# Optimization experiments

Measured on AMD Instinct MI355X. Metric: run time of the kernel, lower is better.

The kernel has to match this reference:

```python
import jax, jax.numpy as jnp
import numpy as np

N_NODES = 100000


def gcn_conv(x, edge_index, W, b, n_nodes):
    """PyG GCNConv: out = D^-1/2 (A + I) D^-1/2 (x @ W^T) + b."""
    src, dst = edge_index[0], edge_index[1]
    loop = jnp.arange(n_nodes, dtype=src.dtype)
    src = jnp.concatenate([src, loop])  # [E + N]
    dst = jnp.concatenate([dst, loop])
    # degree of each node as aggregation target (includes self loop)
    deg = jax.ops.segment_sum(jnp.ones_like(src, dtype=x.dtype), dst,
                              num_segments=n_nodes)
    deg_inv_sqrt = jnp.where(deg > 0, jax.lax.rsqrt(deg), 0.0)
    norm = deg_inv_sqrt[src] * deg_inv_sqrt[dst]  # [E + N]
    h = x @ W.T  # [N, out_dim]  (transform BEFORE propagate, as in PyG)
    msg = h[src] * norm[:, None]  # gather + scale  [E + N, out_dim]
    out = jax.ops.segment_sum(msg, dst, num_segments=n_nodes)  # scatter-add
    return out + b


def setup_inputs() -> dict:
    key = jax.random.key(0)
    k_x, k_e, k_w1, k_b1, k_w2, k_b2 = jax.random.split(key, 6)
    in_dim, hidden = 128, 16
    n_edges = 3200000
    x = jax.random.normal(k_x, (N_NODES, in_dim), dtype=jnp.float32)
    edge_index = jax.random.randint(k_e, (2, n_edges), 0, N_NODES,
                                    dtype=jnp.int64)
    # Glorot-ish init for the linear weights (PyG Linear stores [out, in])
    W1 = jax.random.normal(k_w1, (hidden, in_dim), dtype=jnp.float32) / np.sqrt(in_dim)
    b1 = jnp.zeros((hidden,), dtype=jnp.float32)
    W2 = jax.random.normal(k_w2, (1, hidden), dtype=jnp.float32) / np.sqrt(hidden)
    b2 = jnp.zeros((1,), dtype=jnp.float32)
    return {"x": x, "edge_index": edge_index,
            "W1": W1, "b1": b1, "W2": W2, "b2": b2}


def reference(x, edge_index, W1, b1, W2, b2):
    n = x.shape[0]
    h = jax.nn.relu(gcn_conv(x, edge_index, W1, b1, n))  # [N, hidden]
    out = gcn_conv(h, edge_index, W2, b2, n)  # [N, 1]
    return out.squeeze(-1)  # [N]
```

## Files before the change

kernel.cpp:

```cpp
#include <hip/hip_runtime.h>

#define IN_DIM 128
#define HID 16
#define BSHIFT 7
#define BMASK  127
#define BCAP   4864
#define MID    2432
#define PCH    8192
#define PTHR   512
#define EPT    (PCH / PTHR)
#define BTHR   512
#define TSCALE 4096.0f
#define ZSCALE 262144.0f

__global__ void init_kernel(const unsigned int* ei, int* flag, int* gcur) {
    int tid = blockIdx.x * blockDim.x + threadIdx.x;
    if (tid < 4096) gcur[tid] = 0;
    if (tid == 0) {
        int zeros = 0;
        for (int j = 0; j < 8; ++j)
            if (ei[2 * j + 1] == 0u) zeros++;
        *flag = (zeros >= 7) ? 1 : 0;
    }
}

__device__ __forceinline__ int edge_at(const void* ei, long long idx, int is64) {
    if (is64) return (int)((const long long*)ei)[idx];
    return ((const int*)ei)[idx];
}

__global__ __launch_bounds__(PTHR) void place_kernel(const void* ei, long long E,
        int* gcur, unsigned int* __restrict__ binned, int NB, const int* flag) {
    __shared__ int cnt[1024];
    __shared__ int wbase[1024];
    int tid = threadIdx.x;
    for (int i = tid; i < NB; i += PTHR) cnt[i] = 0;
    __syncthreads();
    const int is64 = *flag;
    const long long e0 = (long long)blockIdx.x * PCH;

    int sA[EPT], dA[EPT];
    if (e0 + PCH <= E) {
        if (is64) {
            const long long* p = (const long long*)ei;
#pragma unroll
            for (int j = 0; j < EPT; ++j) sA[j] = (int)p[e0 + j * PTHR + tid];
#pragma unroll
            for (int j = 0; j < EPT; ++j) dA[j] = (int)p[E + e0 + j * PTHR + tid];
        } else {
            const int* p = (const int*)ei;
#pragma unroll
            for (int j = 0; j < EPT; ++j) sA[j] = p[e0 + j * PTHR + tid];
#pragma unroll
            for (int j = 0; j < EPT; ++j) dA[j] = p[E + e0 + j * PTHR + tid];
        }
    } else {
#pragma unroll
        for (int j = 0; j < EPT; ++j) {
            long long e = e0 + j * PTHR + tid;
            bool ok = e < E;
            sA[j] = ok ? edge_at(ei, e, is64) : 0;
            dA[j] = ok ? edge_at(ei, E + e, is64) : -(BMASK + 1);
        }
    }

    unsigned int v[EPT];
    unsigned int br[EPT];
#pragma unroll
    for (int j = 0; j < EPT; ++j) {
        int b = dA[j] >> BSHIFT;
        bool ok = dA[j] >= 0;
        int r = ok ? atomicAdd(&cnt[b], 1) : 0;
        v[j]  = ((unsigned int)sA[j] << BSHIFT) | (unsigned int)(dA[j] & BMASK);
        br[j] = ok ? (((unsigned int)b << 16) | (unsigned int)r) : 0xFFFFFFFFu;
    }
    __syncthreads();
    const int q = (int)(blockIdx.x & 3);
    int* gc = gcur + q * 1024;
    for (int i = tid; i < NB; i += PTHR) {
        int c = cnt[i];
        wbase[i] = c ? atomicAdd(&gc[i], c) : 0;
    }
    __syncthreads();
    const int regBase = (q >> 1) * MID;
    const bool down = (q & 1);
#pragma unroll
    for (int j = 0; j < EPT; ++j) {
        if (br[j] != 0xFFFFFFFFu) {
            int b = (int)(br[j] >> 16);
            int r = (int)(br[j] & 0xFFFFu);
            int w = wbase[b] + r;
            if (w < MID) {
                int pos = regBase + (down ? (MID - 1 - w) : w);
                binned[(size_t)b * BCAP + pos] = v[j];
            }
        }
    }
}

__device__ __forceinline__ void bucket_ranges(const int* gcur, int b,
        int& r0hi, int& r1lo, int& r1hi, int& r2lo) {
    int cA = gcur[b];            if (cA > MID) cA = MID;
    int cB = gcur[1024 + b];     if (cB > MID - cA) cB = MID - cA;
    int cC = gcur[2048 + b];     if (cC > MID) cC = MID;
    int cD = gcur[3072 + b];     if (cD > MID - cC) cD = MID - cC;
    r0hi = cA;
    r1lo = MID - cB;
    r1hi = MID + cC;
    r2lo = BCAP - cD;
}

__global__ __launch_bounds__(BTHR) void degdis_kernel(
        const unsigned int* __restrict__ binned, const int* __restrict__ gcur,
        float* __restrict__ dis, int N) {
    __shared__ int cnt[128];
    int b = blockIdx.x, tid = threadIdx.x;
    int base = b * BCAP;
    int r0hi, r1lo, r1hi, r2lo;
    bucket_ranges(gcur, b, r0hi, r1lo, r1hi, r2lo);
    if (tid < 128) cnt[tid] = 0;
    __syncthreads();
    for (int e = tid; e < r0hi; e += BTHR)
        atomicAdd(&cnt[binned[(size_t)base + e] & BMASK], 1);
    for (int e = r1lo + tid; e < r1hi; e += BTHR)
        atomicAdd(&cnt[binned[(size_t)base + e] & BMASK], 1);
    for (int e = r2lo + tid; e < BCAP; e += BTHR)
        atomicAdd(&cnt[binned[(size_t)base + e] & BMASK], 1);
    __syncthreads();
    if (tid < 128) {
        int node = (b << BSHIFT) + tid;
        if (node < N) dis[node] = rsqrtf((float)(cnt[tid] + 1));
    }
}

__global__ __launch_bounds__(256) void gemm1_kernel(
        const float* __restrict__ x, const float* __restrict__ W1,
        const float* __restrict__ dis, short* __restrict__ ts16, int N) {
    __shared__ float red[4 * 64 * 17];
    const int tid = threadIdx.x;
    const int lane = tid & 63;
    const int wv = tid >> 6;
    const int wq = __builtin_amdgcn_readfirstlane(wv);
    const int n = blockIdx.x * 64 + lane;

    float acc[HID];
#pragma unroll
    for (int o = 0; o < HID; ++o) acc[o] = 0.f;

    if (n < N) {
        const float* xp = &x[(size_t)n * IN_DIM + wq * 32];
        float4 xv[8];
#pragma unroll
        for (int j = 0; j < 8; ++j) xv[j] = ((const float4*)xp)[j];
        const float* wp = &W1[wq * 32];
#pragma unroll
        for (int kk = 0; kk < 32; ++kk) {
            float xs = ((const float*)xv)[kk];
#pragma unroll
            for (int o = 0; o < HID; ++o)
                acc[o] = fmaf(xs, wp[(size_t)o * IN_DIM + kk], acc[o]);
        }
    }
#pragma unroll
    for (int o = 0; o < HID; ++o)
        red[(wv * 64 + lane) * 17 + o] = acc[o];
    __syncthreads();

    const int nl = tid >> 2;
    const int og = (tid & 3) * 4;
    const int nn = blockIdx.x * 64 + nl;
    if (nn < N) {
        float s0 = 0.f, s1 = 0.f, s2 = 0.f, s3 = 0.f;
#pragma unroll
        for (int w2 = 0; w2 < 4; ++w2) {
            const float* rp = &red[(w2 * 64 + nl) * 17 + og];
            s0 += rp[0]; s1 += rp[1]; s2 += rp[2]; s3 += rp[3];
        }
        float di = dis[nn] * TSCALE;
        int i0 = (int)rintf(fminf(fmaxf(di * s0, -32767.f), 32767.f));
        int i1 = (int)rintf(fminf(fmaxf(di * s1, -32767.f), 32767.f));
        int i2 = (int)rintf(fminf(fmaxf(di * s2, -32767.f), 32767.f));
        int i3 = (int)rintf(fminf(fmaxf(di * s3, -32767.f), 32767.f));
        uint2 pk;
        pk.x = ((unsigned int)i0 & 0xFFFFu) | ((unsigned int)i1 << 16);
        pk.y = ((unsigned int)i2 & 0xFFFFu) | ((unsigned int)i3 << 16);
        ((uint2*)ts16)[(size_t)nn * 4 + (tid & 3)] = pk;
    }
}

__global__ __launch_bounds__(BTHR) void agg1_kernel(
        const unsigned int* __restrict__ binned, const int* __restrict__ gcur,
        const short* __restrict__ ts16, const float* __restrict__ dis,
        const float* __restrict__ b1, const float* __restrict__ W2,
        float* __restrict__ zs, int N) {
    __shared__ int acc[128 * 17];
    int b = blockIdx.x, tid = threadIdx.x;
    for (int i = tid; i < 128 * 17; i += BTHR) acc[i] = 0;
    __syncthreads();
    int base = b * BCAP;
    int r0hi, r1lo, r1hi, r2lo;
    bucket_ranges(gcur, b, r0hi, r1lo, r1hi, r2lo);

#define AGG1_EDGE(IDX)                                                        \
    {                                                                         \
        unsigned int v = binned[(size_t)base + (IDX)];                        \
        int src = (int)(v >> BSHIFT);                                         \
        int row = (int)(v & BMASK) * 17;                                      \
        const int4* tp = (const int4*)(ts16 + (size_t)src * 16);              \
        int4 a = tp[0], c = tp[1];                                            \
        atomicAdd(&acc[row + 0],  (int)(short)(a.x & 0xFFFF));                \
        atomicAdd(&acc[row + 1],  a.x >> 16);                                 \
        atomicAdd(&acc[row + 2],  (int)(short)(a.y & 0xFFFF));                \
        atomicAdd(&acc[row + 3],  a.y >> 16);                                 \
        atomicAdd(&acc[row + 4],  (int)(short)(a.z & 0xFFFF));                \
        atomicAdd(&acc[row + 5],  a.z >> 16);                                 \
        atomicAdd(&acc[row + 6],  (int)(short)(a.w & 0xFFFF));                \
        atomicAdd(&acc[row + 7],  a.w >> 16);                                 \
        atomicAdd(&acc[row + 8],  (int)(short)(c.x & 0xFFFF));                \
        atomicAdd(&acc[row + 9],  c.x >> 16);                                 \
        atomicAdd(&acc[row + 10], (int)(short)(c.y & 0xFFFF));                \
        atomicAdd(&acc[row + 11], c.y >> 16);                                 \
        atomicAdd(&acc[row + 12], (int)(short)(c.z & 0xFFFF));                \
        atomicAdd(&acc[row + 13], c.z >> 16);                                 \
        atomicAdd(&acc[row + 14], (int)(short)(c.w & 0xFFFF));                \
        atomicAdd(&acc[row + 15], c.w >> 16);                                 \
    }

    for (int e = tid; e < r0hi; e += BTHR) AGG1_EDGE(e)
    for (int e = r1lo + tid; e < r1hi; e += BTHR) AGG1_EDGE(e)
    for (int e = r2lo + tid; e < BCAP; e += BTHR) AGG1_EDGE(e)
#undef AGG1_EDGE
    __syncthreads();
    if (tid < 128) {
        int node = (b << BSHIFT) + tid;
        if (node < N) {
            float di = dis[node];
            const int4* tp = (const int4*)(ts16 + (size_t)node * 16);
            int4 a = tp[0], c = tp[1];
            int self[16] = {
                (int)(short)(a.x & 0xFFFF), a.x >> 16,
                (int)(short)(a.y & 0xFFFF), a.y >> 16,
                (int)(short)(a.z & 0xFFFF), a.z >> 16,
                (int)(short)(a.w & 0xFFFF), a.w >> 16,
                (int)(short)(c.x & 0xFFFF), c.x >> 16,
                (int)(short)(c.y & 0xFFFF), c.y >> 16,
                (int)(short)(c.z & 0xFFFF), c.z >> 16,
                (int)(short)(c.w & 0xFFFF), c.w >> 16 };
            float z = 0.f;
#pragma unroll
            for (int j = 0; j < 16; ++j) {
                float s = (float)(acc[tid * 17 + j] + self[j]) * (1.0f / TSCALE);
                float h = fmaxf(fmaf(di, s, b1[j]), 0.f);
                z = fmaf(h, W2[j], z);
            }
            zs[node] = di * z;
        }
    }
}

__global__ __launch_bounds__(BTHR) void agg2_kernel(
        const unsigned int* __restrict__ binned, const int* __restrict__ gcur,
        const float* __restrict__ zs, const float* __restrict__ dis,
        const float* __restrict__ b2, float* __restrict__ out, int N) {
    __shared__ int acc2[128];
    int b = blockIdx.x, tid = threadIdx.x;
    if (tid < 128) acc2[tid] = 0;
    __syncthreads();
    int base = b * BCAP;
    int r0hi, r1lo, r1hi, r2lo;
    bucket_ranges(gcur, b, r0hi, r1lo, r1hi, r2lo);
    for (int e = tid; e < r0hi; e += BTHR) {
        unsigned int v = binned[(size_t)base + e];
        atomicAdd(&acc2[v & BMASK], (int)rintf(zs[v >> BSHIFT] * ZSCALE));
    }
    for (int e = r1lo + tid; e < r1hi; e += BTHR) {
        unsigned int v = binned[(size_t)base + e];
        atomicAdd(&acc2[v & BMASK], (int)rintf(zs[v >> BSHIFT] * ZSCALE));
    }
    for (int e = r2lo + tid; e < BCAP; e += BTHR) {
        unsigned int v = binned[(size_t)base + e];
        atomicAdd(&acc2[v & BMASK], (int)rintf(zs[v >> BSHIFT] * ZSCALE));
    }
    __syncthreads();
    if (tid < 128) {
        int node = (b << BSHIFT) + tid;
        if (node < N) {
            float s = (float)acc2[tid] * (1.0f / ZSCALE) + zs[node];
            out[node] = fmaf(dis[node], s, b2[0]);
        }
    }
}

extern "C" void kernel_launch(void* const* d_in, const int* in_sizes, int n_in,
                              void* d_out, int out_size, void* d_ws, size_t ws_size,
                              hipStream_t stream) {
    const float* x  = (const float*)d_in[0];
    const void*  ei = d_in[1];
    const float* W1 = (const float*)d_in[2];
    const float* b1 = (const float*)d_in[3];
    const float* W2 = (const float*)d_in[4];
    const float* b2 = (const float*)d_in[5];
    float* out = (float*)d_out;

    const int N = in_sizes[0] / IN_DIM;
    const long long E = in_sizes[1] / 2;
    const int NB = (N + BMASK) >> BSHIFT;

    char* w = (char*)d_ws;
    unsigned int* binned = (unsigned int*)w;  w += (size_t)NB * BCAP * sizeof(unsigned int);
    short* ts16   = (short*)w;  w += (size_t)N * HID * sizeof(short);
    float* zs     = (float*)w;  w += (size_t)N * sizeof(float);
    float* dis    = (float*)w;  w += (size_t)N * sizeof(float);
    int*   gcur   = (int*)w;    w += 4096 * sizeof(int);
    int*   flag   = (int*)w;

    init_kernel<<<16, 256, 0, stream>>>((const unsigned int*)ei, flag, gcur);

    int pblk = (int)((E + PCH - 1) / PCH);
    place_kernel<<<pblk, PTHR, 0, stream>>>(ei, E, gcur, binned, NB, flag);

    degdis_kernel<<<NB, BTHR, 0, stream>>>(binned, gcur, dis, N);

    int gblk = (N + 63) / 64;
    gemm1_kernel<<<gblk, 256, 0, stream>>>(x, W1, dis, ts16, N);

    agg1_kernel<<<NB, BTHR, 0, stream>>>(binned, gcur, ts16, dis, b1, W2, zs, N);

    agg2_kernel<<<NB, BTHR, 0, stream>>>(binned, gcur, zs, dis, b2, out, N);
}
```

Before: 97.58 us.

## Fuse degree, GEMM, and two aggregations into one cooperative persistent kernel

```diff
diff --git a/kernel.cpp b/kernel.cpp
--- a/kernel.cpp
+++ b/kernel.cpp
@@ -1,4 +1,6 @@
 #include <hip/hip_runtime.h>
+#include <hip/hip_cooperative_groups.h>
+namespace cg = cooperative_groups;
 
 #define IN_DIM 128
 #define HID 16
@@ -9,7 +11,7 @@
 #define PCH    8192
 #define PTHR   512
 #define EPT    (PCH / PTHR)
-#define BTHR   512
+#define FTHR   256
 #define TSCALE 4096.0f
 #define ZSCALE 262144.0f
 
@@ -110,183 +112,146 @@
     r2lo = BCAP - cD;
 }
 
-__global__ __launch_bounds__(BTHR) void degdis_kernel(
+__global__ __launch_bounds__(FTHR, 4) void fused_kernel(
         const unsigned int* __restrict__ binned, const int* __restrict__ gcur,
-        float* __restrict__ dis, int N) {
+        const float* __restrict__ x, const float* __restrict__ W1,
+        const float* __restrict__ b1, const float* __restrict__ W2,
+        const float* __restrict__ b2, short* __restrict__ ts16,
+        float* __restrict__ zs, float* __restrict__ out, int N) {
+    __shared__ unsigned int eb[BCAP];
+    __shared__ int iacc[128 * 17];
     __shared__ int cnt[128];
-    int b = blockIdx.x, tid = threadIdx.x;
-    int base = b * BCAP;
+    __shared__ float disl[128];
+    __shared__ float zsl[128];
+
+    cg::grid_group grid = cg::this_grid();
+    const int b = blockIdx.x;
+    const int tid = threadIdx.x;
+    const size_t base = (size_t)b * BCAP;
+
     int r0hi, r1lo, r1hi, r2lo;
     bucket_ranges(gcur, b, r0hi, r1lo, r1hi, r2lo);
+    const int len0 = r0hi, len1 = r1hi - r1lo, len2 = BCAP - r2lo;
+    const int total = len0 + len1 + len2;
     if (tid < 128) cnt[tid] = 0;
-    __syncthreads();
-    for (int e = tid; e < r0hi; e += BTHR)
-        atomicAdd(&cnt[binned[(size_t)base + e] & BMASK], 1);
-    for (int e = r1lo + tid; e < r1hi; e += BTHR)
-        atomicAdd(&cnt[binned[(size_t)base + e] & BMASK], 1);
-    for (int e = r2lo + tid; e < BCAP; e += BTHR)
-        atomicAdd(&cnt[binned[(size_t)base + e] & BMASK], 1);
-    __syncthreads();
-    if (tid < 128) {
-        int node = (b << BSHIFT) + tid;
-        if (node < N) dis[node] = rsqrtf((float)(cnt[tid] + 1));
-    }
-}
-
-__global__ __launch_bounds__(256) void gemm1_kernel(
-        const float* __restrict__ x, const float* __restrict__ W1,
-        const float* __restrict__ dis, short* __restrict__ ts16, int N) {
-    __shared__ float red[4 * 64 * 17];
-    const int tid = threadIdx.x;
-    const int lane = tid & 63;
-    const int wv = tid >> 6;
-    const int wq = __builtin_amdgcn_readfirstlane(wv);
-    const int n = blockIdx.x * 64 + lane;
-
-    float acc[HID];
-#pragma unroll
-    for (int o = 0; o < HID; ++o) acc[o] = 0.f;
-
-    if (n < N) {
-        const float* xp = &x[(size_t)n * IN_DIM + wq * 32];
-        float4 xv[8];
-#pragma unroll
-        for (int j = 0; j < 8; ++j) xv[j] = ((const float4*)xp)[j];
+    for (int i = tid; i < 128 * 17; i += FTHR) iacc[i] = 0;
+    __syncthreads();
+    for (int i = tid; i < total; i += FTHR) {
+        int si = (i < len0) ? i
+               : (i < len0 + len1 ? (r1lo + i - len0) : (r2lo + i - len0 - len1));
+        unsigned int v = binned[base + si];
+        eb[i] = v;
+        atomicAdd(&cnt[v & BMASK], 1);
+    }
+    __syncthreads();
+    if (tid < 128) disl[tid] = rsqrtf((float)(cnt[tid] + 1));
+    __syncthreads();
+
+    {
+        const int w = tid >> 6;
+        const int l = tid & 63;
+        const int wq = __builtin_amdgcn_readfirstlane(w);
         const float* wp = &W1[wq * 32];
 #pragma unroll
-        for (int kk = 0; kk < 32; ++kk) {
-            float xs = ((const float*)xv)[kk];
-#pragma unroll
-            for (int o = 0; o < HID; ++o)
-                acc[o] = fmaf(xs, wp[(size_t)o * IN_DIM + kk], acc[o]);
-        }
-    }
-#pragma unroll
-    for (int o = 0; o < HID; ++o)
-        red[(wv * 64 + lane) * 17 + o] = acc[o];
-    __syncthreads();
-
-    const int nl = tid >> 2;
-    const int og = (tid & 3) * 4;
-    const int nn = blockIdx.x * 64 + nl;
-    if (nn < N) {
-        float s0 = 0.f, s1 = 0.f, s2 = 0.f, s3 = 0.f;
-#pragma unroll
-        for (int w2 = 0; w2 < 4; ++w2) {
-            const float* rp = &red[(w2 * 64 + nl) * 17 + og];
-            s0 += rp[0]; s1 += rp[1]; s2 += rp[2]; s3 += rp[3];
-        }
-        float di = dis[nn] * TSCALE;
-        int i0 = (int)rintf(fminf(fmaxf(di * s0, -32767.f), 32767.f));
-        int i1 = (int)rintf(fminf(fmaxf(di * s1, -32767.f), 32767.f));
-        int i2 = (int)rintf(fminf(fmaxf(di * s2, -32767.f), 32767.f));
-        int i3 = (int)rintf(fminf(fmaxf(di * s3, -32767.f), 32767.f));
-        uint2 pk;
-        pk.x = ((unsigned int)i0 & 0xFFFFu) | ((unsigned int)i1 << 16);
-        pk.y = ((unsigned int)i2 & 0xFFFFu) | ((unsigned int)i3 << 16);
-        ((uint2*)ts16)[(size_t)nn * 4 + (tid & 3)] = pk;
-    }
-}
-
-__global__ __launch_bounds__(BTHR) void agg1_kernel(
-        const unsigned int* __restrict__ binned, const int* __restrict__ gcur,
-        const short* __restrict__ ts16, const float* __restrict__ dis,
-        const float* __restrict__ b1, const float* __restrict__ W2,
-        float* __restrict__ zs, int N) {
-    __shared__ int acc[128 * 17];
-    int b = blockIdx.x, tid = threadIdx.x;
-    for (int i = tid; i < 128 * 17; i += BTHR) acc[i] = 0;
-    __syncthreads();
-    int base = b * BCAP;
-    int r0hi, r1lo, r1hi, r2lo;
-    bucket_ranges(gcur, b, r0hi, r1lo, r1hi, r2lo);
-
-#define AGG1_EDGE(IDX)                                                        \
-    {                                                                         \
-        unsigned int v = binned[(size_t)base + (IDX)];                        \
-        int src = (int)(v >> BSHIFT);                                         \
-        int row = (int)(v & BMASK) * 17;                                      \
-        const int4* tp = (const int4*)(ts16 + (size_t)src * 16);              \
-        int4 a = tp[0], c = tp[1];                                            \
-        atomicAdd(&acc[row + 0],  (int)(short)(a.x & 0xFFFF));                \
-        atomicAdd(&acc[row + 1],  a.x >> 16);                                 \
-        atomicAdd(&acc[row + 2],  (int)(short)(a.y & 0xFFFF));                \
-        atomicAdd(&acc[row + 3],  a.y >> 16);                                 \
-        atomicAdd(&acc[row + 4],  (int)(short)(a.z & 0xFFFF));                \
-        atomicAdd(&acc[row + 5],  a.z >> 16);                                 \
-        atomicAdd(&acc[row + 6],  (int)(short)(a.w & 0xFFFF));                \
-        atomicAdd(&acc[row + 7],  a.w >> 16);                                 \
-        atomicAdd(&acc[row + 8],  (int)(short)(c.x & 0xFFFF));                \
-        atomicAdd(&acc[row + 9],  c.x >> 16);                                 \
-        atomicAdd(&acc[row + 10], (int)(short)(c.y & 0xFFFF));                \
-        atomicAdd(&acc[row + 11], c.y >> 16);                                 \
-        atomicAdd(&acc[row + 12], (int)(short)(c.z & 0xFFFF));                \
-        atomicAdd(&acc[row + 13], c.z >> 16);                                 \
-        atomicAdd(&acc[row + 14], (int)(short)(c.w & 0xFFFF));                \
-        atomicAdd(&acc[row + 15], c.w >> 16);                                 \
-    }
-
-    for (int e = tid; e < r0hi; e += BTHR) AGG1_EDGE(e)
-    for (int e = r1lo + tid; e < r1hi; e += BTHR) AGG1_EDGE(e)
-    for (int e = r2lo + tid; e < BCAP; e += BTHR) AGG1_EDGE(e)
-#undef AGG1_EDGE
+        for (int rep = 0; rep < 2; ++rep) {
+            int nl = l + rep * 64;
+            int node = (b << BSHIFT) + nl;
+            if (node < N) {
+                const float* xp = &x[(size_t)node * IN_DIM + wq * 32];
+                float4 xv[8];
+#pragma unroll
+                for (int j = 0; j < 8; ++j) xv[j] = ((const float4*)xp)[j];
+                float acc[HID];
+#pragma unroll
+                for (int o = 0; o < HID; ++o) acc[o] = 0.f;
+#pragma unroll
+                for (int kk = 0; kk < 32; ++kk) {
+                    float xs = ((const float*)xv)[kk];
+#pragma unroll
+                    for (int o = 0; o < HID; ++o)
+                        acc[o] = fmaf(xs, wp[(size_t)o * IN_DIM + kk], acc[o]);
+                }
+                float di = disl[nl] * TSCALE;
+#pragma unroll
+                for (int o = 0; o < HID; ++o)
+                    atomicAdd(&iacc[nl * 17 + o], (int)rintf(di * acc[o]));
+            }
+        }
+    }
+    __syncthreads();
+    {
+        int nl = tid >> 1, part = tid & 1;
+        int node = (b << BSHIFT) + nl;
+        if (nl < 128 && node < N) {
+            int4 pk;
+            int* pkp = (int*)&pk;
+#pragma unroll
+            for (int j = 0; j < 4; ++j) {
+                int v0 = iacc[nl * 17 + part * 8 + 2 * j];
+                int v1 = iacc[nl * 17 + part * 8 + 2 * j + 1];
+                v0 = min(max(v0, -32767), 32767);
+                v1 = min(max(v1, -32767), 32767);
+                pkp[j] = (v0 & 0xFFFF) | (v1 << 16);
+            }
+            ((int4*)ts16)[(size_t)node * 2 + part] = pk;
+        }
+    }
+    grid.sync();
+
+    for (int e = tid; e < total; e += FTHR) {
+        unsigned int v = eb[e];
+        int src = (int)(v >> BSHIFT);
+        int row = (int)(v & BMASK) * 17;
+        const int4* tp = (const int4*)(ts16 + (size_t)src * 16);
+        int4 a = tp[0], c = tp[1];
+        atomicAdd(&iacc[row + 0],  (int)(short)(a.x & 0xFFFF));
+        atomicAdd(&iacc[row + 1],  a.x >> 16);
+        atomicAdd(&iacc[row + 2],  (int)(short)(a.y & 0xFFFF));
+        atomicAdd(&iacc[row + 3],  a.y >> 16);
+        atomicAdd(&iacc[row + 4],  (int)(short)(a.z & 0xFFFF));
+        atomicAdd(&iacc[row + 5],  a.z >> 16);
+        atomicAdd(&iacc[row + 6],  (int)(short)(a.w & 0xFFFF));
+        atomicAdd(&iacc[row + 7],  a.w >> 16);
+        atomicAdd(&iacc[row + 8],  (int)(short)(c.x & 0xFFFF));
+        atomicAdd(&iacc[row + 9],  c.x >> 16);
+        atomicAdd(&iacc[row + 10], (int)(short)(c.y & 0xFFFF));
+        atomicAdd(&iacc[row + 11], c.y >> 16);
+        atomicAdd(&iacc[row + 12], (int)(short)(c.z & 0xFFFF));
+        atomicAdd(&iacc[row + 13], c.z >> 16);
+        atomicAdd(&iacc[row + 14], (int)(short)(c.w & 0xFFFF));
+        atomicAdd(&iacc[row + 15], c.w >> 16);
+    }
     __syncthreads();
     if (tid < 128) {
         int node = (b << BSHIFT) + tid;
         if (node < N) {
-            float di = dis[node];
-            const int4* tp = (const int4*)(ts16 + (size_t)node * 16);
-            int4 a = tp[0], c = tp[1];
-            int self[16] = {
-                (int)(short)(a.x & 0xFFFF), a.x >> 16,
-                (int)(short)(a.y & 0xFFFF), a.y >> 16,
-                (int)(short)(a.z & 0xFFFF), a.z >> 16,
-                (int)(short)(a.w & 0xFFFF), a.w >> 16,
-                (int)(short)(c.x & 0xFFFF), c.x >> 16,
-                (int)(short)(c.y & 0xFFFF), c.y >> 16,
-                (int)(short)(c.z & 0xFFFF), c.z >> 16,
-                (int)(short)(c.w & 0xFFFF), c.w >> 16 };
+            float di = disl[tid];
             float z = 0.f;
 #pragma unroll
             for (int j = 0; j < 16; ++j) {
-                float s = (float)(acc[tid * 17 + j] + self[j]) * (1.0f / TSCALE);
+                float s = (float)iacc[tid * 17 + j] * (1.0f / TSCALE);
                 float h = fmaxf(fmaf(di, s, b1[j]), 0.f);
                 z = fmaf(h, W2[j], z);
             }
-            zs[node] = di * z;
-        }
-    }
-}
-
-__global__ __launch_bounds__(BTHR) void agg2_kernel(
-        const unsigned int* __restrict__ binned, const int* __restrict__ gcur,
-        const float* __restrict__ zs, const float* __restrict__ dis,
-        const float* __restrict__ b2, float* __restrict__ out, int N) {
-    __shared__ int acc2[128];
-    int b = blockIdx.x, tid = threadIdx.x;
-    if (tid < 128) acc2[tid] = 0;
-    __syncthreads();
-    int base = b * BCAP;
-    int r0hi, r1lo, r1hi, r2lo;
-    bucket_ranges(gcur, b, r0hi, r1lo, r1hi, r2lo);
-    for (int e = tid; e < r0hi; e += BTHR) {
-        unsigned int v = binned[(size_t)base + e];
-        atomicAdd(&acc2[v & BMASK], (int)rintf(zs[v >> BSHIFT] * ZSCALE));
-    }
-    for (int e = r1lo + tid; e < r1hi; e += BTHR) {
-        unsigned int v = binned[(size_t)base + e];
-        atomicAdd(&acc2[v & BMASK], (int)rintf(zs[v >> BSHIFT] * ZSCALE));
-    }
-    for (int e = r2lo + tid; e < BCAP; e += BTHR) {
-        unsigned int v = binned[(size_t)base + e];
-        atomicAdd(&acc2[v & BMASK], (int)rintf(zs[v >> BSHIFT] * ZSCALE));
+            float zv = di * z;
+            zsl[tid] = zv;
+            zs[node] = zv;
+        }
+    }
+    grid.sync();
+
+    if (tid < 128) cnt[tid] = 0;
+    __syncthreads();
+    for (int e = tid; e < total; e += FTHR) {
+        unsigned int v = eb[e];
+        atomicAdd(&cnt[v & BMASK], (int)rintf(zs[v >> BSHIFT] * ZSCALE));
     }
     __syncthreads();
     if (tid < 128) {
         int node = (b << BSHIFT) + tid;
         if (node < N) {
-            float s = (float)acc2[tid] * (1.0f / ZSCALE) + zs[node];
-            out[node] = fmaf(dis[node], s, b2[0]);
+            float s = (float)cnt[tid] * (1.0f / ZSCALE) + zsl[tid];
+            out[node] = fmaf(disl[tid], s, b2[0]);
         }
     }
 }
@@ -302,7 +267,7 @@
     const float* b2 = (const float*)d_in[5];
     float* out = (float*)d_out;
 
-    const int N = in_sizes[0] / IN_DIM;
+    int N = in_sizes[0] / IN_DIM;
     const long long E = in_sizes[1] / 2;
     const int NB = (N + BMASK) >> BSHIFT;
 
@@ -310,7 +275,6 @@
     unsigned int* binned = (unsigned int*)w;  w += (size_t)NB * BCAP * sizeof(unsigned int);
     short* ts16   = (short*)w;  w += (size_t)N * HID * sizeof(short);
     float* zs     = (float*)w;  w += (size_t)N * sizeof(float);
-    float* dis    = (float*)w;  w += (size_t)N * sizeof(float);
     int*   gcur   = (int*)w;    w += 4096 * sizeof(int);
     int*   flag   = (int*)w;
 
@@ -319,12 +283,9 @@
     int pblk = (int)((E + PCH - 1) / PCH);
     place_kernel<<<pblk, PTHR, 0, stream>>>(ei, E, gcur, binned, NB, flag);
 
-    degdis_kernel<<<NB, BTHR, 0, stream>>>(binned, gcur, dis, N);
-
-    int gblk = (N + 63) / 64;
-    gemm1_kernel<<<gblk, 256, 0, stream>>>(x, W1, dis, ts16, N);
-
-    agg1_kernel<<<NB, BTHR, 0, stream>>>(binned, gcur, ts16, dis, b1, W2, zs, N);
-
-    agg2_kernel<<<NB, BTHR, 0, stream>>>(binned, gcur, zs, dis, b2, out, N);
-}
+    void* kargs[] = { (void*)&binned, (void*)&gcur, (void*)&x, (void*)&W1,
+                      (void*)&b1, (void*)&W2, (void*)&b2, (void*)&ts16,
+                      (void*)&zs, (void*)&out, (void*)&N };
+    hipLaunchCooperativeKernel((const void*)fused_kernel, dim3(NB), dim3(FTHR),
+                               kargs, 0, stream);
+}
```

After: 286.0 us. 193% more time.
